# Kernel tuning notes

Hardware: AMD Instinct MI355X
Metric: run time of the kernel (lower is better)

## Reference

```python
import jax, jax.numpy as jnp
import numpy as np

N = 210          # sequence length (== module max_length cap)
DM = 2048        # input feature dim (major and minor)
DK = 1024        # key/query dim
DV = 1024        # value dim
K_CLIP = 32      # relative-position clipping distance


def _make_table(n, k):
    # table[i, j] = clip(j - i, -k, k) + k  (Shaw-style relative position index)
    rel = np.arange(n)[None, :] - np.arange(n)[:, None]
    return jnp.asarray(np.clip(rel, -k, k) + k, dtype=jnp.int32)


def setup_inputs() -> dict:
    key = jax.random.key(0)
    ks = jax.random.split(key, 7)
    X_major = jax.random.normal(ks[0], (N, DM), dtype=jnp.float32)
    X_minor = jax.random.normal(ks[1], (N, DM), dtype=jnp.float32)
    # Linear weights stored as [in, out] for x @ W
    s = 0.02
    Wq = jax.random.normal(ks[2], (DM, DK), dtype=jnp.float32) * s
    Wk = jax.random.normal(ks[3], (DM, DK), dtype=jnp.float32) * s
    Wv = jax.random.normal(ks[4], (DM, DV), dtype=jnp.float32) * s
    Wo = jax.random.normal(ks[5], (DV, DV), dtype=jnp.float32) * s
    wk = jax.random.normal(ks[6], (2 * K_CLIP + 1, DK), dtype=jnp.float32) * s
    table = _make_table(N, K_CLIP)
    return {"X_major": X_major, "X_minor": X_minor, "Wq": Wq, "Wk": Wk,
            "Wv": Wv, "Wo": Wo, "wk": wk, "table": table}


def reference(X_major, X_minor, Wq, Wk, Wv, Wo, wk, table):
    n = X_major.shape[0]
    scale = 1.0 / jnp.sqrt(jnp.asarray(Wq.shape[1], X_major.dtype))
    Q = X_major @ Wq                     # [n, dk]
    K = X_minor @ Wk                     # [n, dk]
    V = X_minor @ Wv                     # [n, dv]
    Qs = Q * scale
    S = Qs @ K.T                         # [n, n] content scores
    Rk = wk[table[:n, :n]]               # [n, n, dk] gathered rel-pos reps
    Sr = jnp.einsum('id,ijd->ij', Qs, Rk)  # [n, n] relative scores
    A = jax.nn.softmax(S + Sr, axis=-1)  # [n, n]
    Y = (A @ V) @ Wo                     # [n, dv]
    return (Y, A)
```

## Files before the change

kernel.cpp:

```cpp
#include <hip/hip_runtime.h>

typedef short bf16x8 __attribute__((ext_vector_type(8)));
typedef float f32x4 __attribute__((ext_vector_type(4)));

#define MFMA16(a, b, c) __builtin_amdgcn_mfma_f32_16x16x32_bf16(a, b, c, 0, 0, 0)

__device__ inline short f2bf(float f) {
  unsigned u = __builtin_bit_cast(unsigned, f);
  u += 0x7FFFu + ((u >> 16) & 1u);
  return (short)(u >> 16);
}
__device__ inline unsigned pack2(float lo, float hi) {
  unsigned a = __builtin_bit_cast(unsigned, lo) + 0x8000u;
  unsigned b = __builtin_bit_cast(unsigned, hi) + 0x8000u;
  return __builtin_amdgcn_perm(b, a, 0x07060302u);
}

__device__ inline void async_cp16(const void* g, void* l) {
  __builtin_amdgcn_global_load_lds(
      (const __attribute__((address_space(1))) unsigned int*)g,
      (__attribute__((address_space(3))) unsigned int*)l, 16, 0, 0);
}

#define SWZ(r, c) ((((r) << 4) + ((c) ^ ((r) & 7))) << 3)


__global__ __launch_bounds__(256) void k_prep(const float* __restrict__ xmaj,
                                              const float* __restrict__ xmin,
                                              const float* __restrict__ wkin,
                                              const float* __restrict__ Wq,
                                              const float* __restrict__ Wk,
                                              const float* __restrict__ Wv,
                                              const float* __restrict__ Wo,
                                              short* __restrict__ xmaj_bf,
                                              short* __restrict__ xmin_bf,
                                              short* __restrict__ kwb,
                                              short* __restrict__ wqt,
                                              short* __restrict__ wkt,
                                              short* __restrict__ wvt,
                                              short* __restrict__ wot) {
  __shared__ short tile[64][72];
  int b = blockIdx.x, t = threadIdx.x;
  if (b < 512) {
    int idx = b * 256 + t;
    if (idx < 107520) {
      float4 v = ((const float4*)xmaj)[idx];
      ((uint2*)xmaj_bf)[idx] = make_uint2(pack2(v.x, v.y), pack2(v.z, v.w));
      float4 u = ((const float4*)xmin)[idx];
      ((uint2*)xmin_bf)[idx] = make_uint2(pack2(u.x, u.y), pack2(u.z, u.w));
    }
    if (idx < 16640) {
      float4 v = ((const float4*)wkin)[idx];
      ((uint2*)(kwb + 210 * 1024))[idx] = make_uint2(pack2(v.x, v.y), pack2(v.z, v.w));
    }
    if (idx < 1664) ((uint4*)(kwb + 275 * 1024))[idx] = make_uint4(0, 0, 0, 0);
    return;
  }
  const float* W;
  short* Wt;
  int kt, nt, dstK;
  if (b < 2048) {
    int wi = (b - 512) >> 9, tl = (b - 512) & 511;
    W = wi == 0 ? Wq : (wi == 1 ? Wk : Wv);
    Wt = wi == 0 ? wqt : (wi == 1 ? wkt : wvt);
    kt = tl >> 4; nt = tl & 15; dstK = 2048;
  } else {
    int tl = b - 2048;
    W = Wo; Wt = wot; kt = tl >> 4; nt = tl & 15; dstK = 1024;
  }
  int k0 = kt * 64, n0 = nt * 64;
  int kp = t >> 4, nl4 = (t & 15) * 4;
  for (int h = 0; h < 2; ++h) {
    int kpp = kp + h * 16;
    const float* g = W + (size_t)(k0 + 2 * kpp) * 1024 + n0 + nl4;
    float4 u = *(const float4*)g;
    float4 v = *(const float4*)(g + 1024);
    *(unsigned*)&tile[nl4 + 0][2 * kpp] = pack2(u.x, v.x);
    *(unsigned*)&tile[nl4 + 1][2 * kpp] = pack2(u.y, v.y);
    *(unsigned*)&tile[nl4 + 2][2 * kpp] = pack2(u.z, v.z);
    *(unsigned*)&tile[nl4 + 3][2 * kpp] = pack2(u.w, v.w);
  }
  __syncthreads();
  int nl = t >> 2, cq = t & 3;
  for (int h = 0; h < 2; ++h) {
    int c = cq + h * 4;
    *(uint4*)(Wt + (size_t)(n0 + nl) * dstK + k0 + c * 8) = *(const uint4*)&tile[nl][c * 8];
  }
}

__global__ __launch_bounds__(256, 1) void k_qkv(const short* __restrict__ xmaj,
                                                const short* __restrict__ xmin,
                                                const short* __restrict__ wqt,
                                                const short* __restrict__ wkt,
                                                const short* __restrict__ wvt,
                                                short* __restrict__ qs,
                                                short* __restrict__ kwb,
                                                short* __restrict__ vt) {
  __shared__ short As[64 * 128];
  __shared__ short Bs[64 * 128];
  int b = blockIdx.x, t = threadIdx.x;
  int x = b & 7, s = b >> 3;
  int ntile = x * 6 + (s >> 2), mtile = s & 3;
  int nn0 = ntile * 64;
  int mat = nn0 >> 10, ncol0 = nn0 & 1023, m0 = mtile * 64;
  const short* A = (mat == 0) ? xmaj : xmin;
  const short* Bt = (mat == 0) ? wqt : (mat == 1 ? wkt : wvt);
  int lane = t & 63, w = t >> 6;
  int wm = w >> 1, wn = w & 1;
  int l15 = lane & 15, l4 = lane >> 4;
  f32x4 acc[2][2] = {};

  for (int k0 = 0; k0 < 2048; k0 += 128) {
    __syncthreads();
#pragma unroll
    for (int j = 0; j < 4; ++j) {
      int sj = t + j * 256;
      int r = sj >> 4, cg = (sj & 15) ^ (r & 7);
      async_cp16(A + (size_t)(m0 + r) * 2048 + k0 + cg * 8, &As[(w * 64 + j * 256) * 8]);
    }
#pragma unroll
    for (int j = 0; j < 4; ++j) {
      int sj = t + j * 256;
      int r = sj >> 4, cg = (sj & 15) ^ (r & 7);
      async_cp16(Bt + (size_t)(ncol0 + r) * 2048 + k0 + cg * 8, &Bs[(w * 64 + j * 256) * 8]);
    }
    __syncthreads();
#pragma unroll
    for (int kk = 0; kk < 4; ++kk) {
      int c = kk * 4 + l4;
      int ra0 = wm * 32 + l15, ra1 = ra0 + 16;
      int rb0 = wn * 32 + l15, rb1 = rb0 + 16;
      bf16x8 a0 = *(const bf16x8*)&As[SWZ(ra0, c)];
      bf16x8 a1 = *(const bf16x8*)&As[SWZ(ra1, c)];
      bf16x8 b0 = *(const bf16x8*)&Bs[SWZ(rb0, c)];
      bf16x8 b1 = *(const bf16x8*)&Bs[SWZ(rb1, c)];
      acc[0][0] = MFMA16(a0, b0, acc[0][0]);
      acc[0][1] = MFMA16(a0, b1, acc[0][1]);
      acc[1][0] = MFMA16(a1, b0, acc[1][0]);
      acc[1][1] = MFMA16(a1, b1, acc[1][1]);
    }
  }

  if (mat < 2) {
    float scale = (mat == 0) ? 0.03125f : 1.0f;
    short* dst = (mat == 0) ? qs : kwb;
#pragma unroll
    for (int mi = 0; mi < 2; ++mi)
#pragma unroll
      for (int ni = 0; ni < 2; ++ni) {
        int r0 = m0 + wm * 32 + mi * 16 + l4 * 4;
        int c = ncol0 + wn * 32 + ni * 16 + l15;
        for (int j = 0; j < 4; ++j) {
          int r = r0 + j;
          if (r < 210) dst[r * 1024 + c] = f2bf(acc[mi][ni][j] * scale);
        }
      }
  } else {
    __syncthreads();
#pragma unroll
    for (int mi = 0; mi < 2; ++mi)
#pragma unroll
      for (int ni = 0; ni < 2; ++ni) {
        int nl = wn * 32 + ni * 16 + l15;
        int ml0 = wm * 32 + mi * 16 + l4 * 4;
        for (int j = 0; j < 4; ++j) As[nl * 72 + ml0 + j] = f2bf(acc[mi][ni][j]);
      }
    __syncthreads();
    for (int h = 0; h < 2; ++h) {
      int idx = t + h * 256;
      int nl = idx >> 3, c8 = idx & 7;
      int mg0 = m0 + c8 * 8;
      short* dstp = vt + (ncol0 + nl) * 256 + mg0;
      if (mg0 + 8 <= 210) {
        *(uint4*)dstp = *(const uint4*)&As[nl * 72 + c8 * 8];
      } else {
        for (int e = 0; e < 8; ++e)
          if (mg0 + e < 210) dstp[e] = As[nl * 72 + c8 * 8 + e];
      }
    }
  }
}

__global__ __launch_bounds__(256, 1) void k_sprime(const short* __restrict__ qs,
                                                   const short* __restrict__ kwb,
                                                   float* __restrict__ Sp) {
  __shared__ short As[32 * 128];
  __shared__ short Bs[64 * 128];
  int n0 = blockIdx.x * 64, m0 = blockIdx.y * 32;
  int t = threadIdx.x, lane = t & 63, w = t >> 6;
  int l15 = lane & 15, l4 = lane >> 4;
  f32x4 acc[2] = {};

  for (int k0 = 0; k0 < 1024; k0 += 128) {
    __syncthreads();
#pragma unroll
    for (int j = 0; j < 2; ++j) {
      int sj = t + j * 256;
      int r = sj >> 4, cg = (sj & 15) ^ (r & 7);
      async_cp16(qs + (size_t)(m0 + r) * 1024 + k0 + cg * 8, &As[(w * 64 + j * 256) * 8]);
    }
#pragma unroll
    for (int j = 0; j < 4; ++j) {
      int sj = t + j * 256;
      int r = sj >> 4, cg = (sj & 15) ^ (r & 7);
      async_cp16(kwb + (size_t)(n0 + r) * 1024 + k0 + cg * 8, &Bs[(w * 64 + j * 256) * 8]);
    }
    __syncthreads();
#pragma unroll
    for (int kk = 0; kk < 4; ++kk) {
      int c = kk * 4 + l4;
      int rb = w * 16 + l15;
      bf16x8 a0 = *(const bf16x8*)&As[SWZ(l15, c)];
      bf16x8 a1 = *(const bf16x8*)&As[SWZ(16 + l15, c)];
      bf16x8 bb = *(const bf16x8*)&Bs[SWZ(rb, c)];
      acc[0] = MFMA16(a0, bb, acc[0]);
      acc[1] = MFMA16(a1, bb, acc[1]);
    }
  }
#pragma unroll
  for (int mi = 0; mi < 2; ++mi) {
    int r0 = m0 + mi * 16 + l4 * 4;
    int col = n0 + w * 16 + l15;
    for (int j = 0; j < 4; ++j) Sp[(r0 + j) * 320 + col] = acc[mi][j];
  }
}

__global__ __launch_bounds__(256) void k_softmax(const float* __restrict__ Sp,
                                                 const int* __restrict__ table,
                                                 short* __restrict__ Abf,
                                                 float* __restrict__ outA) {
  int i = blockIdx.x, t = threadIdx.x;
  if (i >= 210) {
    Abf[i * 256 + t] = 0;
    return;
  }
  __shared__ float srow[288];
  __shared__ float red[4];
  for (int j = t; j < 288; j += 256) srow[j] = Sp[i * 320 + j];
  __syncthreads();
  float logit = -1e30f;
  if (t < 210) {
    int tb = table[i * 210 + t];
    logit = srow[t] + srow[210 + tb];
  }
  float m = logit;
  for (int o = 32; o; o >>= 1) m = fmaxf(m, __shfl_xor(m, o));
  if ((t & 63) == 0) red[t >> 6] = m;
  __syncthreads();
  m = fmaxf(fmaxf(red[0], red[1]), fmaxf(red[2], red[3]));
  float e = (t < 210) ? __expf(logit - m) : 0.0f;
  float s = e;
  for (int o = 32; o; o >>= 1) s += __shfl_xor(s, o);
  __syncthreads();
  if ((t & 63) == 0) red[t >> 6] = s;
  __syncthreads();
  s = red[0] + red[1] + red[2] + red[3];
  float a = e / s;
  Abf[i * 256 + t] = (t < 210) ? f2bf(a) : (short)0;
  if (t < 210) outA[i * 210 + t] = a;
}

__global__ __launch_bounds__(256, 1) void k_av(const short* __restrict__ Abf,
                                               const short* __restrict__ vt,
                                               short* __restrict__ av) {
  __shared__ short As[64 * 128];
  __shared__ short Bs[64 * 128];
  int n0 = blockIdx.x * 64, m0 = blockIdx.y * 64;
  int t = threadIdx.x, lane = t & 63, w = t >> 6;
  int wm = w >> 1, wn = w & 1;
  int l15 = lane & 15, l4 = lane >> 4;
  f32x4 acc[2][2] = {};

  for (int k0 = 0; k0 < 256; k0 += 128) {
    __syncthreads();
#pragma unroll
    for (int j = 0; j < 4; ++j) {
      int sj = t + j * 256;
      int r = sj >> 4, cg = (sj & 15) ^ (r & 7);
      async_cp16(Abf + (size_t)(m0 + r) * 256 + k0 + cg * 8, &As[(w * 64 + j * 256) * 8]);
      async_cp16(vt + (size_t)(n0 + r) * 256 + k0 + cg * 8, &Bs[(w * 64 + j * 256) * 8]);
    }
    __syncthreads();
#pragma unroll
    for (int kk = 0; kk < 4; ++kk) {
      int c = kk * 4 + l4;
      int ra0 = wm * 32 + l15, ra1 = ra0 + 16;
      int rb0 = wn * 32 + l15, rb1 = rb0 + 16;
      bf16x8 a0 = *(const bf16x8*)&As[SWZ(ra0, c)];
      bf16x8 a1 = *(const bf16x8*)&As[SWZ(ra1, c)];
      bf16x8 b0 = *(const bf16x8*)&Bs[SWZ(rb0, c)];
      bf16x8 b1 = *(const bf16x8*)&Bs[SWZ(rb1, c)];
      acc[0][0] = MFMA16(a0, b0, acc[0][0]);
      acc[0][1] = MFMA16(a0, b1, acc[0][1]);
      acc[1][0] = MFMA16(a1, b0, acc[1][0]);
      acc[1][1] = MFMA16(a1, b1, acc[1][1]);
    }
  }
#pragma unroll
  for (int mi = 0; mi < 2; ++mi)
#pragma unroll
    for (int ni = 0; ni < 2; ++ni) {
      int r0 = m0 + wm * 32 + mi * 16 + l4 * 4;
      int c = n0 + wn * 32 + ni * 16 + l15;
      for (int j = 0; j < 4; ++j) {
        int r = r0 + j;
        if (r < 210) av[r * 1024 + c] = f2bf(acc[mi][ni][j]);
      }
    }
}

__global__ __launch_bounds__(256, 1) void k_y(const short* __restrict__ av,
                                              const short* __restrict__ wot,
                                              float* __restrict__ outY) {
  __shared__ short As[64 * 128];
  __shared__ short Bs[64 * 128];
  int n0 = blockIdx.x * 64, m0 = blockIdx.y * 64;
  int t = threadIdx.x, lane = t & 63, w = t >> 6;
  int wm = w >> 1, wn = w & 1;
  int l15 = lane & 15, l4 = lane >> 4;
  f32x4 acc[2][2] = {};

  for (int k0 = 0; k0 < 1024; k0 += 128) {
    __syncthreads();
#pragma unroll
    for (int j = 0; j < 4; ++j) {
      int sj = t + j * 256;
      int r = sj >> 4, cg = (sj & 15) ^ (r & 7);
      async_cp16(av + (size_t)(m0 + r) * 1024 + k0 + cg * 8, &As[(w * 64 + j * 256) * 8]);
      async_cp16(wot + (size_t)(n0 + r) * 1024 + k0 + cg * 8, &Bs[(w * 64 + j * 256) * 8]);
    }
    __syncthreads();
#pragma unroll
    for (int kk = 0; kk < 4; ++kk) {
      int c = kk * 4 + l4;
      int ra0 = wm * 32 + l15, ra1 = ra0 + 16;
      int rb0 = wn * 32 + l15, rb1 = rb0 + 16;
      bf16x8 a0 = *(const bf16x8*)&As[SWZ(ra0, c)];
      bf16x8 a1 = *(const bf16x8*)&As[SWZ(ra1, c)];
      bf16x8 b0 = *(const bf16x8*)&Bs[SWZ(rb0, c)];
      bf16x8 b1 = *(const bf16x8*)&Bs[SWZ(rb1, c)];
      acc[0][0] = MFMA16(a0, b0, acc[0][0]);
      acc[0][1] = MFMA16(a0, b1, acc[0][1]);
      acc[1][0] = MFMA16(a1, b0, acc[1][0]);
      acc[1][1] = MFMA16(a1, b1, acc[1][1]);
    }
  }
#pragma unroll
  for (int mi = 0; mi < 2; ++mi)
#pragma unroll
    for (int ni = 0; ni < 2; ++ni) {
      int r0 = m0 + wm * 32 + mi * 16 + l4 * 4;
      int c = n0 + wn * 32 + ni * 16 + l15;
      for (int j = 0; j < 4; ++j) {
        int r = r0 + j;
        if (r < 210) outY[r * 1024 + c] = acc[mi][ni][j];
      }
    }
}

extern "C" void kernel_launch(void* const* d_in, const int* in_sizes, int n_in,
                              void* d_out, int out_size, void* d_ws, size_t ws_size,
                              hipStream_t stream) {
  const float* Xmaj = (const float*)d_in[0];
  const float* Xmin = (const float*)d_in[1];
  const float* Wq = (const float*)d_in[2];
  const float* Wk = (const float*)d_in[3];
  const float* Wv = (const float*)d_in[4];
  const float* Wo = (const float*)d_in[5];
  const float* wk = (const float*)d_in[6];
  const int* table = (const int*)d_in[7];

  char* ws = (char*)d_ws;
  short* xmaj_bf = (short*)(ws + 0);
  short* xmin_bf = (short*)(ws + 1048576);
  short* qs = (short*)(ws + 2097152);
  short* kwb = (short*)(ws + 2621440);
  short* vt = (short*)(ws + 3276800);
  short* Abf = (short*)(ws + 3801088);
  short* av = (short*)(ws + 3932160);
  float* Sp = (float*)(ws + 4456448);
  short* wqt = (short*)(ws + 4743168);
  short* wkt = (short*)(ws + 8937472);
  short* wvt = (short*)(ws + 13131776);
  short* wot = (short*)(ws + 17326080);

  float* outY = (float*)d_out;
  float* outA = (float*)d_out + 215040;

  k_prep<<<2304, 256, 0, stream>>>(Xmaj, Xmin, wk, Wq, Wk, Wv, Wo,
                                   xmaj_bf, xmin_bf, kwb, wqt, wkt, wvt, wot);
  k_qkv<<<192, 256, 0, stream>>>(xmaj_bf, xmin_bf, wqt, wkt, wvt, qs, kwb, vt);
  k_sprime<<<dim3(5, 7), 256, 0, stream>>>(qs, kwb, Sp);
  k_softmax<<<256, 256, 0, stream>>>(Sp, table, Abf, outA);
  k_av<<<dim3(16, 4), 256, 0, stream>>>(Abf, vt, av);
  k_y<<<dim3(16, 4), 256, 0, stream>>>(av, wot, outY);
}
```

Measured before the change: 127.0 us.

## Fuse all stages into one cooperative persistent kernel with grid syncs

Replaces the six separate kernels with one cooperative kernel of 192 blocks that runs prep, QKV GEMM, scores+softmax, A@V and the output projection, separated by grid-wide syncs. The score GEMM and softmax are merged per 32-row block so scores stay in shared memory instead of going through a global buffer. This is meant to remove kernel launch overhead and inter-kernel gaps. In exchange, the weight conversion/transpose stage runs on far fewer blocks, and later stages leave most blocks idle at barriers.

Result: slower. 257.1 us (+102.4%).

```diff
diff --git a/kernel.cpp b/kernel.cpp
--- a/kernel.cpp
+++ b/kernel.cpp
@@ -1,4 +1,7 @@
 #include <hip/hip_runtime.h>
+#include <hip/hip_cooperative_groups.h>
+
+namespace cg = cooperative_groups;
 
 typedef short bf16x8 __attribute__((ext_vector_type(8)));
 typedef float f32x4 __attribute__((ext_vector_type(4)));
@@ -15,347 +18,352 @@
   unsigned b = __builtin_bit_cast(unsigned, hi) + 0x8000u;
   return __builtin_amdgcn_perm(b, a, 0x07060302u);
 }
-
 __device__ inline void async_cp16(const void* g, void* l) {
   __builtin_amdgcn_global_load_lds(
       (const __attribute__((address_space(1))) unsigned int*)g,
       (__attribute__((address_space(3))) unsigned int*)l, 16, 0, 0);
 }
-
 #define SWZ(r, c) ((((r) << 4) + ((c) ^ ((r) & 7))) << 3)
 
 
-__global__ __launch_bounds__(256) void k_prep(const float* __restrict__ xmaj,
-                                              const float* __restrict__ xmin,
-                                              const float* __restrict__ wkin,
-                                              const float* __restrict__ Wq,
-                                              const float* __restrict__ Wk,
-                                              const float* __restrict__ Wv,
-                                              const float* __restrict__ Wo,
-                                              short* __restrict__ xmaj_bf,
-                                              short* __restrict__ xmin_bf,
-                                              short* __restrict__ kwb,
-                                              short* __restrict__ wqt,
-                                              short* __restrict__ wkt,
-                                              short* __restrict__ wvt,
-                                              short* __restrict__ wot) {
-  __shared__ short tile[64][72];
+__global__ __launch_bounds__(256, 1) void k_fused(const float* __restrict__ xmajf,
+                                                  const float* __restrict__ xminf,
+                                                  const float* __restrict__ Wqf,
+                                                  const float* __restrict__ Wkf,
+                                                  const float* __restrict__ Wvf,
+                                                  const float* __restrict__ Wof,
+                                                  const float* __restrict__ wkin,
+                                                  const int* __restrict__ table,
+                                                  char* __restrict__ ws,
+                                                  float* __restrict__ dout) {
+  __shared__ char smem[90112];
+  cg::grid_group gg = cg::this_grid();
   int b = blockIdx.x, t = threadIdx.x;
-  if (b < 512) {
-    int idx = b * 256 + t;
-    if (idx < 107520) {
-      float4 v = ((const float4*)xmaj)[idx];
-      ((uint2*)xmaj_bf)[idx] = make_uint2(pack2(v.x, v.y), pack2(v.z, v.w));
-      float4 u = ((const float4*)xmin)[idx];
-      ((uint2*)xmin_bf)[idx] = make_uint2(pack2(u.x, u.y), pack2(u.z, u.w));
-    }
-    if (idx < 16640) {
-      float4 v = ((const float4*)wkin)[idx];
-      ((uint2*)(kwb + 210 * 1024))[idx] = make_uint2(pack2(v.x, v.y), pack2(v.z, v.w));
-    }
-    if (idx < 1664) ((uint4*)(kwb + 275 * 1024))[idx] = make_uint4(0, 0, 0, 0);
-    return;
-  }
-  const float* W;
-  short* Wt;
-  int kt, nt, dstK;
-  if (b < 2048) {
-    int wi = (b - 512) >> 9, tl = (b - 512) & 511;
-    W = wi == 0 ? Wq : (wi == 1 ? Wk : Wv);
-    Wt = wi == 0 ? wqt : (wi == 1 ? wkt : wvt);
-    kt = tl >> 4; nt = tl & 15; dstK = 2048;
-  } else {
-    int tl = b - 2048;
-    W = Wo; Wt = wot; kt = tl >> 4; nt = tl & 15; dstK = 1024;
-  }
-  int k0 = kt * 64, n0 = nt * 64;
-  int kp = t >> 4, nl4 = (t & 15) * 4;
-  for (int h = 0; h < 2; ++h) {
-    int kpp = kp + h * 16;
-    const float* g = W + (size_t)(k0 + 2 * kpp) * 1024 + n0 + nl4;
-    float4 u = *(const float4*)g;
-    float4 v = *(const float4*)(g + 1024);
-    *(unsigned*)&tile[nl4 + 0][2 * kpp] = pack2(u.x, v.x);
-    *(unsigned*)&tile[nl4 + 1][2 * kpp] = pack2(u.y, v.y);
-    *(unsigned*)&tile[nl4 + 2][2 * kpp] = pack2(u.z, v.z);
-    *(unsigned*)&tile[nl4 + 3][2 * kpp] = pack2(u.w, v.w);
-  }
-  __syncthreads();
-  int nl = t >> 2, cq = t & 3;
-  for (int h = 0; h < 2; ++h) {
-    int c = cq + h * 4;
-    *(uint4*)(Wt + (size_t)(n0 + nl) * dstK + k0 + c * 8) = *(const uint4*)&tile[nl][c * 8];
-  }
-}
-
-__global__ __launch_bounds__(256, 1) void k_qkv(const short* __restrict__ xmaj,
-                                                const short* __restrict__ xmin,
-                                                const short* __restrict__ wqt,
-                                                const short* __restrict__ wkt,
-                                                const short* __restrict__ wvt,
-                                                short* __restrict__ qs,
-                                                short* __restrict__ kwb,
-                                                short* __restrict__ vt) {
-  __shared__ short As[64 * 128];
-  __shared__ short Bs[64 * 128];
-  int b = blockIdx.x, t = threadIdx.x;
-  int x = b & 7, s = b >> 3;
-  int ntile = x * 6 + (s >> 2), mtile = s & 3;
-  int nn0 = ntile * 64;
-  int mat = nn0 >> 10, ncol0 = nn0 & 1023, m0 = mtile * 64;
-  const short* A = (mat == 0) ? xmaj : xmin;
-  const short* Bt = (mat == 0) ? wqt : (mat == 1 ? wkt : wvt);
   int lane = t & 63, w = t >> 6;
-  int wm = w >> 1, wn = w & 1;
   int l15 = lane & 15, l4 = lane >> 4;
-  f32x4 acc[2][2] = {};
-
-  for (int k0 = 0; k0 < 2048; k0 += 128) {
+
+  short* xmaj_bf = (short*)(ws);
+  short* xmin_bf = (short*)(ws + 1048576);
+  short* qs = (short*)(ws + 2097152);
+  short* kwb = (short*)(ws + 2621440);
+  short* vt = (short*)(ws + 3276800);
+  short* Abf = (short*)(ws + 3801088);
+  short* av = (short*)(ws + 3932160);
+  short* wqt = (short*)(ws + 4743168);
+  short* wkt = (short*)(ws + 8937472);
+  short* wvt = (short*)(ws + 13131776);
+  short* wot = (short*)(ws + 17326080);
+  float* outY = dout;
+  float* outA = dout + 215040;
+
+  {
+    for (int i = b * 256 + t; i < 107520; i += 49152) {
+      float4 v = ((const float4*)xmajf)[i];
+      ((uint2*)xmaj_bf)[i] = make_uint2(pack2(v.x, v.y), pack2(v.z, v.w));
+      float4 u = ((const float4*)xminf)[i];
+      ((uint2*)xmin_bf)[i] = make_uint2(pack2(u.x, u.y), pack2(u.z, u.w));
+    }
+    for (int i = b * 256 + t; i < 16640; i += 49152) {
+      float4 v = ((const float4*)wkin)[i];
+      ((uint2*)(kwb + 210 * 1024))[i] = make_uint2(pack2(v.x, v.y), pack2(v.z, v.w));
+    }
+    for (int i = b * 256 + t; i < 1664; i += 49152)
+      ((uint4*)(kwb + 275 * 1024))[i] = make_uint4(0, 0, 0, 0);
+
+    short(*tile)[72] = (short(*)[72])smem;
+    int kp = t >> 4, nl4 = (t & 15) * 4;
+    int nl = t >> 2, cq = t & 3;
+    for (int tid = b; tid < 1792; tid += 192) {
+      const float* W;
+      short* Wt;
+      int kt, nt, dstK;
+      if (tid < 1536) {
+        int wi = tid >> 9, tl = tid & 511;
+        W = wi == 0 ? Wqf : (wi == 1 ? Wkf : Wvf);
+        Wt = wi == 0 ? wqt : (wi == 1 ? wkt : wvt);
+        kt = tl >> 4; nt = tl & 15; dstK = 2048;
+      } else {
+        int tl = tid - 1536;
+        W = Wof; Wt = wot; kt = tl >> 4; nt = tl & 15; dstK = 1024;
+      }
+      int k0 = kt * 64, n0 = nt * 64;
+      __syncthreads();
+#pragma unroll
+      for (int h = 0; h < 2; ++h) {
+        int kpp = kp + h * 16;
+        const float* g = W + (size_t)(k0 + 2 * kpp) * 1024 + n0 + nl4;
+        float4 u = *(const float4*)g;
+        float4 v = *(const float4*)(g + 1024);
+        *(unsigned*)&tile[nl4 + 0][2 * kpp] = pack2(u.x, v.x);
+        *(unsigned*)&tile[nl4 + 1][2 * kpp] = pack2(u.y, v.y);
+        *(unsigned*)&tile[nl4 + 2][2 * kpp] = pack2(u.z, v.z);
+        *(unsigned*)&tile[nl4 + 3][2 * kpp] = pack2(u.w, v.w);
+      }
+      __syncthreads();
+#pragma unroll
+      for (int h = 0; h < 2; ++h) {
+        int c = cq + h * 4;
+        *(uint4*)(Wt + (size_t)(n0 + nl) * dstK + k0 + c * 8) = *(const uint4*)&tile[nl][c * 8];
+      }
+    }
+  }
+  gg.sync();
+
+  {
+    short* As = (short*)smem;
+    short* Bs = (short*)(smem + 16384);
+    int x = b & 7, s = b >> 3;
+    int ntile = x * 6 + (s >> 2), mtile = s & 3;
+    int nn0 = ntile * 64;
+    int mat = nn0 >> 10, ncol0 = nn0 & 1023, m0 = mtile * 64;
+    const short* A = (mat == 0) ? xmaj_bf : xmin_bf;
+    const short* Bt = (mat == 0) ? wqt : (mat == 1 ? wkt : wvt);
+    int wm = w >> 1, wn = w & 1;
+    f32x4 acc[2][2] = {};
+
+    for (int k0 = 0; k0 < 2048; k0 += 128) {
+      __syncthreads();
+#pragma unroll
+      for (int j = 0; j < 4; ++j) {
+        int sj = t + j * 256;
+        int r = sj >> 4, cg2 = (sj & 15) ^ (r & 7);
+        async_cp16(A + (size_t)(m0 + r) * 2048 + k0 + cg2 * 8, &As[(w * 64 + j * 256) * 8]);
+      }
+#pragma unroll
+      for (int j = 0; j < 4; ++j) {
+        int sj = t + j * 256;
+        int r = sj >> 4, cg2 = (sj & 15) ^ (r & 7);
+        async_cp16(Bt + (size_t)(ncol0 + r) * 2048 + k0 + cg2 * 8, &Bs[(w * 64 + j * 256) * 8]);
+      }
+      __syncthreads();
+#pragma unroll
+      for (int kk = 0; kk < 4; ++kk) {
+        int c = kk * 4 + l4;
+        int ra0 = wm * 32 + l15, ra1 = ra0 + 16;
+        int rb0 = wn * 32 + l15, rb1 = rb0 + 16;
+        bf16x8 a0 = *(const bf16x8*)&As[SWZ(ra0, c)];
+        bf16x8 a1 = *(const bf16x8*)&As[SWZ(ra1, c)];
+        bf16x8 b0 = *(const bf16x8*)&Bs[SWZ(rb0, c)];
+        bf16x8 b1 = *(const bf16x8*)&Bs[SWZ(rb1, c)];
+        acc[0][0] = MFMA16(a0, b0, acc[0][0]);
+        acc[0][1] = MFMA16(a0, b1, acc[0][1]);
+        acc[1][0] = MFMA16(a1, b0, acc[1][0]);
+        acc[1][1] = MFMA16(a1, b1, acc[1][1]);
+      }
+    }
+
+    if (mat < 2) {
+      float scale = (mat == 0) ? 0.03125f : 1.0f;
+      short* dst = (mat == 0) ? qs : kwb;
+#pragma unroll
+      for (int mi = 0; mi < 2; ++mi)
+#pragma unroll
+        for (int ni = 0; ni < 2; ++ni) {
+          int r0 = m0 + wm * 32 + mi * 16 + l4 * 4;
+          int c = ncol0 + wn * 32 + ni * 16 + l15;
+          for (int j = 0; j < 4; ++j) {
+            int r = r0 + j;
+            if (r < 210) dst[r * 1024 + c] = f2bf(acc[mi][ni][j] * scale);
+          }
+        }
+    } else {
+      __syncthreads();
+#pragma unroll
+      for (int mi = 0; mi < 2; ++mi)
+#pragma unroll
+        for (int ni = 0; ni < 2; ++ni) {
+          int nl = wn * 32 + ni * 16 + l15;
+          int ml0 = wm * 32 + mi * 16 + l4 * 4;
+          for (int j = 0; j < 4; ++j) As[nl * 72 + ml0 + j] = f2bf(acc[mi][ni][j]);
+        }
+      __syncthreads();
+      for (int h = 0; h < 2; ++h) {
+        int idx = t + h * 256;
+        int nl = idx >> 3, c8 = idx & 7;
+        int mg0 = m0 + c8 * 8;
+        short* dstp = vt + (ncol0 + nl) * 256 + mg0;
+        if (mg0 + 8 <= 210) {
+          *(uint4*)dstp = *(const uint4*)&As[nl * 72 + c8 * 8];
+        } else {
+          for (int e = 0; e < 8; ++e)
+            if (mg0 + e < 210) dstp[e] = As[nl * 72 + c8 * 8 + e];
+        }
+      }
+    }
+  }
+  gg.sync();
+
+#define SST 292
+  if (b < 7) {
+    short* As2 = (short*)smem;
+    short* Bs2 = (short*)(smem + 8192);
+    float* Ssh = (float*)(smem + 8192);
+    int m0 = b * 32;
+    f32x4 acc[2][5] = {};
+
+    for (int k0 = 0; k0 < 1024; k0 += 128) {
+      __syncthreads();
+#pragma unroll
+      for (int j = 0; j < 2; ++j) {
+        int sj = t + j * 256;
+        int r = sj >> 4, cg2 = (sj & 15) ^ (r & 7);
+        async_cp16(qs + (size_t)(m0 + r) * 1024 + k0 + cg2 * 8, &As2[(w * 64 + j * 256) * 8]);
+      }
+#pragma unroll
+      for (int j = 0; j < 20; ++j) {
+        int sj = t + j * 256;
+        int r = sj >> 4, cg2 = (sj & 15) ^ (r & 7);
+        async_cp16(kwb + (size_t)r * 1024 + k0 + cg2 * 8, &Bs2[(w * 64 + j * 256) * 8]);
+      }
+      __syncthreads();
+#pragma unroll
+      for (int kk = 0; kk < 4; ++kk) {
+        int c = kk * 4 + l4;
+        bf16x8 a0 = *(const bf16x8*)&As2[SWZ(l15, c)];
+        bf16x8 a1 = *(const bf16x8*)&As2[SWZ(16 + l15, c)];
+#pragma unroll
+        for (int ni = 0; ni < 5; ++ni) {
+          bf16x8 bb = *(const bf16x8*)&Bs2[SWZ(w * 80 + ni * 16 + l15, c)];
+          acc[0][ni] = MFMA16(a0, bb, acc[0][ni]);
+          acc[1][ni] = MFMA16(a1, bb, acc[1][ni]);
+        }
+      }
+    }
     __syncthreads();
 #pragma unroll
-    for (int j = 0; j < 4; ++j) {
-      int sj = t + j * 256;
-      int r = sj >> 4, cg = (sj & 15) ^ (r & 7);
-      async_cp16(A + (size_t)(m0 + r) * 2048 + k0 + cg * 8, &As[(w * 64 + j * 256) * 8]);
-    }
-#pragma unroll
-    for (int j = 0; j < 4; ++j) {
-      int sj = t + j * 256;
-      int r = sj >> 4, cg = (sj & 15) ^ (r & 7);
-      async_cp16(Bt + (size_t)(ncol0 + r) * 2048 + k0 + cg * 8, &Bs[(w * 64 + j * 256) * 8]);
-    }
+    for (int mi = 0; mi < 2; ++mi)
+#pragma unroll
+      for (int ni = 0; ni < 5; ++ni) {
+        int col = w * 80 + ni * 16 + l15;
+        if (col < 288) {
+          int r0 = mi * 16 + l4 * 4;
+          for (int jj = 0; jj < 4; ++jj) Ssh[(r0 + jj) * SST + col] = acc[mi][ni][jj];
+        }
+      }
     __syncthreads();
-#pragma unroll
-    for (int kk = 0; kk < 4; ++kk) {
-      int c = kk * 4 + l4;
-      int ra0 = wm * 32 + l15, ra1 = ra0 + 16;
-      int rb0 = wn * 32 + l15, rb1 = rb0 + 16;
-      bf16x8 a0 = *(const bf16x8*)&As[SWZ(ra0, c)];
-      bf16x8 a1 = *(const bf16x8*)&As[SWZ(ra1, c)];
-      bf16x8 b0 = *(const bf16x8*)&Bs[SWZ(rb0, c)];
-      bf16x8 b1 = *(const bf16x8*)&Bs[SWZ(rb1, c)];
-      acc[0][0] = MFMA16(a0, b0, acc[0][0]);
-      acc[0][1] = MFMA16(a0, b1, acc[0][1]);
-      acc[1][0] = MFMA16(a1, b0, acc[1][0]);
-      acc[1][1] = MFMA16(a1, b1, acc[1][1]);
-    }
-  }
-
-  if (mat < 2) {
-    float scale = (mat == 0) ? 0.03125f : 1.0f;
-    short* dst = (mat == 0) ? qs : kwb;
+
+    int r = t >> 3, c = t & 7;
+    int row = m0 + r;
+    float* Sr = Ssh + r * SST;
+    if (row < 210) {
+      const int* tr = table + row * 210;
+      float mx = -1e30f;
+      for (int j = c; j < 210; j += 8) {
+        float lg = Sr[j] + Sr[210 + tr[j]];
+        Sr[j] = lg;
+        mx = fmaxf(mx, lg);
+      }
+      for (int o = 4; o; o >>= 1) mx = fmaxf(mx, __shfl_xor(mx, o, 8));
+      float sum = 0.0f;
+      for (int j = c; j < 210; j += 8) {
+        float e = __expf(Sr[j] - mx);
+        Sr[j] = e;
+        sum += e;
+      }
+      for (int o = 4; o; o >>= 1) sum += __shfl_xor(sum, o, 8);
+      float inv = 1.0f / sum;
+      for (int j = c; j < 210; j += 8) {
+        float a = Sr[j] * inv;
+        outA[row * 210 + j] = a;
+        Abf[row * 256 + j] = f2bf(a);
+      }
+      for (int j = 210 + c; j < 256; j += 8) Abf[row * 256 + j] = 0;
+    } else {
+      for (int j = c; j < 256; j += 8) Abf[row * 256 + j] = 0;
+    }
+  } else if (b == 7) {
+    for (int i = t; i < 1472; i += 256) ((uint4*)(Abf + 210 * 256))[i] = make_uint4(0, 0, 0, 0);
+  }
+  gg.sync();
+
+  if (b < 64) {
+    short* As = (short*)smem;
+    short* Bs = (short*)(smem + 16384);
+    int n0 = (b & 15) * 64, m0 = (b >> 4) * 64;
+    int wm = w >> 1, wn = w & 1;
+    f32x4 acc[2][2] = {};
+    for (int k0 = 0; k0 < 256; k0 += 128) {
+      __syncthreads();
+#pragma unroll
+      for (int j = 0; j < 4; ++j) {
+        int sj = t + j * 256;
+        int r = sj >> 4, cg2 = (sj & 15) ^ (r & 7);
+        async_cp16(Abf + (size_t)(m0 + r) * 256 + k0 + cg2 * 8, &As[(w * 64 + j * 256) * 8]);
+        async_cp16(vt + (size_t)(n0 + r) * 256 + k0 + cg2 * 8, &Bs[(w * 64 + j * 256) * 8]);
+      }
+      __syncthreads();
+#pragma unroll
+      for (int kk = 0; kk < 4; ++kk) {
+        int c = kk * 4 + l4;
+        int ra0 = wm * 32 + l15, ra1 = ra0 + 16;
+        int rb0 = wn * 32 + l15, rb1 = rb0 + 16;
+        bf16x8 a0 = *(const bf16x8*)&As[SWZ(ra0, c)];
+        bf16x8 a1 = *(const bf16x8*)&As[SWZ(ra1, c)];
+        bf16x8 b0 = *(const bf16x8*)&Bs[SWZ(rb0, c)];
+        bf16x8 b1 = *(const bf16x8*)&Bs[SWZ(rb1, c)];
+        acc[0][0] = MFMA16(a0, b0, acc[0][0]);
+        acc[0][1] = MFMA16(a0, b1, acc[0][1]);
+        acc[1][0] = MFMA16(a1, b0, acc[1][0]);
+        acc[1][1] = MFMA16(a1, b1, acc[1][1]);
+      }
+    }
 #pragma unroll
     for (int mi = 0; mi < 2; ++mi)
 #pragma unroll
       for (int ni = 0; ni < 2; ++ni) {
         int r0 = m0 + wm * 32 + mi * 16 + l4 * 4;
-        int c = ncol0 + wn * 32 + ni * 16 + l15;
+        int c = n0 + wn * 32 + ni * 16 + l15;
         for (int j = 0; j < 4; ++j) {
           int r = r0 + j;
-          if (r < 210) dst[r * 1024 + c] = f2bf(acc[mi][ni][j] * scale);
-        }
-      }
-  } else {
-    __syncthreads();
+          if (r < 210) av[r * 1024 + c] = f2bf(acc[mi][ni][j]);
+        }
+      }
+  }
+  gg.sync();
+
+  if (b < 64) {
+    short* As = (short*)smem;
+    short* Bs = (short*)(smem + 16384);
+    int n0 = (b & 15) * 64, m0 = (b >> 4) * 64;
+    int wm = w >> 1, wn = w & 1;
+    f32x4 acc[2][2] = {};
+    for (int k0 = 0; k0 < 1024; k0 += 128) {
+      __syncthreads();
+#pragma unroll
+      for (int j = 0; j < 4; ++j) {
+        int sj = t + j * 256;
+        int r = sj >> 4, cg2 = (sj & 15) ^ (r & 7);
+        async_cp16(av + (size_t)(m0 + r) * 1024 + k0 + cg2 * 8, &As[(w * 64 + j * 256) * 8]);
+        async_cp16(wot + (size_t)(n0 + r) * 1024 + k0 + cg2 * 8, &Bs[(w * 64 + j * 256) * 8]);
+      }
+      __syncthreads();
+#pragma unroll
+      for (int kk = 0; kk < 4; ++kk) {
+        int c = kk * 4 + l4;
+        int ra0 = wm * 32 + l15, ra1 = ra0 + 16;
+        int rb0 = wn * 32 + l15, rb1 = rb0 + 16;
+        bf16x8 a0 = *(const bf16x8*)&As[SWZ(ra0, c)];
+        bf16x8 a1 = *(const bf16x8*)&As[SWZ(ra1, c)];
+        bf16x8 b0 = *(const bf16x8*)&Bs[SWZ(rb0, c)];
+        bf16x8 b1 = *(const bf16x8*)&Bs[SWZ(rb1, c)];
+        acc[0][0] = MFMA16(a0, b0, acc[0][0]);
+        acc[0][1] = MFMA16(a0, b1, acc[0][1]);
+        acc[1][0] = MFMA16(a1, b0, acc[1][0]);
+        acc[1][1] = MFMA16(a1, b1, acc[1][1]);
+      }
+    }
 #pragma unroll
     for (int mi = 0; mi < 2; ++mi)
 #pragma unroll
       for (int ni = 0; ni < 2; ++ni) {
-        int nl = wn * 32 + ni * 16 + l15;
-        int ml0 = wm * 32 + mi * 16 + l4 * 4;
-        for (int j = 0; j < 4; ++j) As[nl * 72 + ml0 + j] = f2bf(acc[mi][ni][j]);
-      }
-    __syncthreads();
-    for (int h = 0; h < 2; ++h) {
-      int idx = t + h * 256;
-      int nl = idx >> 3, c8 = idx & 7;
-      int mg0 = m0 + c8 * 8;
-      short* dstp = vt + (ncol0 + nl) * 256 + mg0;
-      if (mg0 + 8 <= 210) {
-        *(uint4*)dstp = *(const uint4*)&As[nl * 72 + c8 * 8];
-      } else {
-        for (int e = 0; e < 8; ++e)
-          if (mg0 + e < 210) dstp[e] = As[nl * 72 + c8 * 8 + e];
-      }
-    }
-  }
-}
-
-__global__ __launch_bounds__(256, 1) void k_sprime(const short* __restrict__ qs,
-                                                   const short* __restrict__ kwb,
-                                                   float* __restrict__ Sp) {
-  __shared__ short As[32 * 128];
-  __shared__ short Bs[64 * 128];
-  int n0 = blockIdx.x * 64, m0 = blockIdx.y * 32;
-  int t = threadIdx.x, lane = t & 63, w = t >> 6;
-  int l15 = lane & 15, l4 = lane >> 4;
-  f32x4 acc[2] = {};
-
-  for (int k0 = 0; k0 < 1024; k0 += 128) {
-    __syncthreads();
-#pragma unroll
-    for (int j = 0; j < 2; ++j) {
-      int sj = t + j * 256;
-      int r = sj >> 4, cg = (sj & 15) ^ (r & 7);
-      async_cp16(qs + (size_t)(m0 + r) * 1024 + k0 + cg * 8, &As[(w * 64 + j * 256) * 8]);
-    }
-#pragma unroll
-    for (int j = 0; j < 4; ++j) {
-      int sj = t + j * 256;
-      int r = sj >> 4, cg = (sj & 15) ^ (r & 7);
-      async_cp16(kwb + (size_t)(n0 + r) * 1024 + k0 + cg * 8, &Bs[(w * 64 + j * 256) * 8]);
-    }
-    __syncthreads();
-#pragma unroll
-    for (int kk = 0; kk < 4; ++kk) {
-      int c = kk * 4 + l4;
-      int rb = w * 16 + l15;
-      bf16x8 a0 = *(const bf16x8*)&As[SWZ(l15, c)];
-      bf16x8 a1 = *(const bf16x8*)&As[SWZ(16 + l15, c)];
-      bf16x8 bb = *(const bf16x8*)&Bs[SWZ(rb, c)];
-      acc[0] = MFMA16(a0, bb, acc[0]);
-      acc[1] = MFMA16(a1, bb, acc[1]);
-    }
-  }
-#pragma unroll
-  for (int mi = 0; mi < 2; ++mi) {
-    int r0 = m0 + mi * 16 + l4 * 4;
-    int col = n0 + w * 16 + l15;
-    for (int j = 0; j < 4; ++j) Sp[(r0 + j) * 320 + col] = acc[mi][j];
-  }
-}
-
-__global__ __launch_bounds__(256) void k_softmax(const float* __restrict__ Sp,
-                                                 const int* __restrict__ table,
-                                                 short* __restrict__ Abf,
-                                                 float* __restrict__ outA) {
-  int i = blockIdx.x, t = threadIdx.x;
-  if (i >= 210) {
-    Abf[i * 256 + t] = 0;
-    return;
-  }
-  __shared__ float srow[288];
-  __shared__ float red[4];
-  for (int j = t; j < 288; j += 256) srow[j] = Sp[i * 320 + j];
-  __syncthreads();
-  float logit = -1e30f;
-  if (t < 210) {
-    int tb = table[i * 210 + t];
-    logit = srow[t] + srow[210 + tb];
-  }
-  float m = logit;
-  for (int o = 32; o; o >>= 1) m = fmaxf(m, __shfl_xor(m, o));
-  if ((t & 63) == 0) red[t >> 6] = m;
-  __syncthreads();
-  m = fmaxf(fmaxf(red[0], red[1]), fmaxf(red[2], red[3]));
-  float e = (t < 210) ? __expf(logit - m) : 0.0f;
-  float s = e;
-  for (int o = 32; o; o >>= 1) s += __shfl_xor(s, o);
-  __syncthreads();
-  if ((t & 63) == 0) red[t >> 6] = s;
-  __syncthreads();
-  s = red[0] + red[1] + red[2] + red[3];
-  float a = e / s;
-  Abf[i * 256 + t] = (t < 210) ? f2bf(a) : (short)0;
-  if (t < 210) outA[i * 210 + t] = a;
-}
-
-__global__ __launch_bounds__(256, 1) void k_av(const short* __restrict__ Abf,
-                                               const short* __restrict__ vt,
-                                               short* __restrict__ av) {
-  __shared__ short As[64 * 128];
-  __shared__ short Bs[64 * 128];
-  int n0 = blockIdx.x * 64, m0 = blockIdx.y * 64;
-  int t = threadIdx.x, lane = t & 63, w = t >> 6;
-  int wm = w >> 1, wn = w & 1;
-  int l15 = lane & 15, l4 = lane >> 4;
-  f32x4 acc[2][2] = {};
-
-  for (int k0 = 0; k0 < 256; k0 += 128) {
-    __syncthreads();
-#pragma unroll
-    for (int j = 0; j < 4; ++j) {
-      int sj = t + j * 256;
-      int r = sj >> 4, cg = (sj & 15) ^ (r & 7);
-      async_cp16(Abf + (size_t)(m0 + r) * 256 + k0 + cg * 8, &As[(w * 64 + j * 256) * 8]);
-      async_cp16(vt + (size_t)(n0 + r) * 256 + k0 + cg * 8, &Bs[(w * 64 + j * 256) * 8]);
-    }
-    __syncthreads();
-#pragma unroll
-    for (int kk = 0; kk < 4; ++kk) {
-      int c = kk * 4 + l4;
-      int ra0 = wm * 32 + l15, ra1 = ra0 + 16;
-      int rb0 = wn * 32 + l15, rb1 = rb0 + 16;
-      bf16x8 a0 = *(const bf16x8*)&As[SWZ(ra0, c)];
-      bf16x8 a1 = *(const bf16x8*)&As[SWZ(ra1, c)];
-      bf16x8 b0 = *(const bf16x8*)&Bs[SWZ(rb0, c)];
-      bf16x8 b1 = *(const bf16x8*)&Bs[SWZ(rb1, c)];
-      acc[0][0] = MFMA16(a0, b0, acc[0][0]);
-      acc[0][1] = MFMA16(a0, b1, acc[0][1]);
-      acc[1][0] = MFMA16(a1, b0, acc[1][0]);
-      acc[1][1] = MFMA16(a1, b1, acc[1][1]);
-    }
-  }
-#pragma unroll
-  for (int mi = 0; mi < 2; ++mi)
-#pragma unroll
-    for (int ni = 0; ni < 2; ++ni) {
-      int r0 = m0 + wm * 32 + mi * 16 + l4 * 4;
-      int c = n0 + wn * 32 + ni * 16 + l15;
-      for (int j = 0; j < 4; ++j) {
-        int r = r0 + j;
-        if (r < 210) av[r * 1024 + c] = f2bf(acc[mi][ni][j]);
-      }
-    }
-}
-
-__global__ __launch_bounds__(256, 1) void k_y(const short* __restrict__ av,
-                                              const short* __restrict__ wot,
-                                              float* __restrict__ outY) {
-  __shared__ short As[64 * 128];
-  __shared__ short Bs[64 * 128];
-  int n0 = blockIdx.x * 64, m0 = blockIdx.y * 64;
-  int t = threadIdx.x, lane = t & 63, w = t >> 6;
-  int wm = w >> 1, wn = w & 1;
-  int l15 = lane & 15, l4 = lane >> 4;
-  f32x4 acc[2][2] = {};
-
-  for (int k0 = 0; k0 < 1024; k0 += 128) {
-    __syncthreads();
-#pragma unroll
-    for (int j = 0; j < 4; ++j) {
-      int sj = t + j * 256;
-      int r = sj >> 4, cg = (sj & 15) ^ (r & 7);
-      async_cp16(av + (size_t)(m0 + r) * 1024 + k0 + cg * 8, &As[(w * 64 + j * 256) * 8]);
-      async_cp16(wot + (size_t)(n0 + r) * 1024 + k0 + cg * 8, &Bs[(w * 64 + j * 256) * 8]);
-    }
-    __syncthreads();
-#pragma unroll
-    for (int kk = 0; kk < 4; ++kk) {
-      int c = kk * 4 + l4;
-      int ra0 = wm * 32 + l15, ra1 = ra0 + 16;
-      int rb0 = wn * 32 + l15, rb1 = rb0 + 16;
-      bf16x8 a0 = *(const bf16x8*)&As[SWZ(ra0, c)];
-      bf16x8 a1 = *(const bf16x8*)&As[SWZ(ra1, c)];
-      bf16x8 b0 = *(const bf16x8*)&Bs[SWZ(rb0, c)];
-      bf16x8 b1 = *(const bf16x8*)&Bs[SWZ(rb1, c)];
-      acc[0][0] = MFMA16(a0, b0, acc[0][0]);
-      acc[0][1] = MFMA16(a0, b1, acc[0][1]);
-      acc[1][0] = MFMA16(a1, b0, acc[1][0]);
-      acc[1][1] = MFMA16(a1, b1, acc[1][1]);
-    }
-  }
-#pragma unroll
-  for (int mi = 0; mi < 2; ++mi)
-#pragma unroll
-    for (int ni = 0; ni < 2; ++ni) {
-      int r0 = m0 + wm * 32 + mi * 16 + l4 * 4;
-      int c = n0 + wn * 32 + ni * 16 + l15;
-      for (int j = 0; j < 4; ++j) {
-        int r = r0 + j;
-        if (r < 210) outY[r * 1024 + c] = acc[mi][ni][j];
-      }
-    }
+        int r0 = m0 + wm * 32 + mi * 16 + l4 * 4;
+        int c = n0 + wn * 32 + ni * 16 + l15;
+        for (int j = 0; j < 4; ++j) {
+          int r = r0 + j;
+          if (r < 210) outY[r * 1024 + c] = acc[mi][ni][j];
+        }
+      }
+  }
 }
 
 extern "C" void kernel_launch(void* const* d_in, const int* in_sizes, int n_in,
@@ -369,29 +377,10 @@
   const float* Wo = (const float*)d_in[5];
   const float* wk = (const float*)d_in[6];
   const int* table = (const int*)d_in[7];
-
-  char* ws = (char*)d_ws;
-  short* xmaj_bf = (short*)(ws + 0);
-  short* xmin_bf = (short*)(ws + 1048576);
-  short* qs = (short*)(ws + 2097152);
-  short* kwb = (short*)(ws + 2621440);
-  short* vt = (short*)(ws + 3276800);
-  short* Abf = (short*)(ws + 3801088);
-  short* av = (short*)(ws + 3932160);
-  float* Sp = (float*)(ws + 4456448);
-  short* wqt = (short*)(ws + 4743168);
-  short* wkt = (short*)(ws + 8937472);
-  short* wvt = (short*)(ws + 13131776);
-  short* wot = (short*)(ws + 17326080);
-
-  float* outY = (float*)d_out;
-  float* outA = (float*)d_out + 215040;
-
-  k_prep<<<2304, 256, 0, stream>>>(Xmaj, Xmin, wk, Wq, Wk, Wv, Wo,
-                                   xmaj_bf, xmin_bf, kwb, wqt, wkt, wvt, wot);
-  k_qkv<<<192, 256, 0, stream>>>(xmaj_bf, xmin_bf, wqt, wkt, wvt, qs, kwb, vt);
-  k_sprime<<<dim3(5, 7), 256, 0, stream>>>(qs, kwb, Sp);
-  k_softmax<<<256, 256, 0, stream>>>(Sp, table, Abf, outA);
-  k_av<<<dim3(16, 4), 256, 0, stream>>>(Abf, vt, av);
-  k_y<<<dim3(16, 4), 256, 0, stream>>>(av, wot, outY);
-}
+  char* wsp = (char*)d_ws;
+  float* outp = (float*)d_out;
+
+  void* args[] = {(void*)&Xmaj, (void*)&Xmin, (void*)&Wq, (void*)&Wk, (void*)&Wv,
+                  (void*)&Wo,   (void*)&wk,   (void*)&table, (void*)&wsp, (void*)&outp};
+  hipLaunchCooperativeKernel((void*)k_fused, dim3(192), dim3(256), args, 0, stream);
+}
```

## Fuse score GEMM and softmax into one attention kernel

Applied to the files above, without the earlier changes.

Merges the S' GEMM (Q against K and relative-position keys) with the row softmax into a single kernel. Each of 7 blocks computes a full 32x320 score strip in LDS and applies the softmax there, so the Sp buffer round trip through global memory and one kernel launch go away. Zeroing of the padding rows of Abf moves into the prep kernel. The cost is far less parallelism: 7 blocks instead of 35 for the GEMM, and each block must stream all of kwb by itself.

After: 146.1 us. 15.0% more time.

```diff
diff --git a/kernel.cpp b/kernel.cpp
--- a/kernel.cpp
+++ b/kernel.cpp
@@ -35,6 +35,7 @@
                                               short* __restrict__ xmaj_bf,
                                               short* __restrict__ xmin_bf,
                                               short* __restrict__ kwb,
+                                              short* __restrict__ Abf,
                                               short* __restrict__ wqt,
                                               short* __restrict__ wkt,
                                               short* __restrict__ wvt,
@@ -54,6 +55,8 @@
       ((uint2*)(kwb + 210 * 1024))[idx] = make_uint2(pack2(v.x, v.y), pack2(v.z, v.w));
     }
     if (idx < 1664) ((uint4*)(kwb + 275 * 1024))[idx] = make_uint4(0, 0, 0, 0);
+    if (idx < 1472)
+      ((uint4*)(Abf + 210 * 256))[idx] = make_uint4(0, 0, 0, 0);
     return;
   }
   const float* W;
@@ -181,83 +184,91 @@
   }
 }
 
-__global__ __launch_bounds__(256, 1) void k_sprime(const short* __restrict__ qs,
-                                                   const short* __restrict__ kwb,
-                                                   float* __restrict__ Sp) {
-  __shared__ short As[32 * 128];
-  __shared__ short Bs[64 * 128];
-  int n0 = blockIdx.x * 64, m0 = blockIdx.y * 32;
-  int t = threadIdx.x, lane = t & 63, w = t >> 6;
-  int l15 = lane & 15, l4 = lane >> 4;
-  f32x4 acc[2] = {};
-
-  for (int k0 = 0; k0 < 1024; k0 += 128) {
-    __syncthreads();
-#pragma unroll
-    for (int j = 0; j < 2; ++j) {
-      int sj = t + j * 256;
-      int r = sj >> 4, cg = (sj & 15) ^ (r & 7);
-      async_cp16(qs + (size_t)(m0 + r) * 1024 + k0 + cg * 8, &As[(w * 64 + j * 256) * 8]);
-    }
-#pragma unroll
-    for (int j = 0; j < 4; ++j) {
-      int sj = t + j * 256;
-      int r = sj >> 4, cg = (sj & 15) ^ (r & 7);
-      async_cp16(kwb + (size_t)(n0 + r) * 1024 + k0 + cg * 8, &Bs[(w * 64 + j * 256) * 8]);
-    }
-    __syncthreads();
-#pragma unroll
-    for (int kk = 0; kk < 4; ++kk) {
-      int c = kk * 4 + l4;
-      int rb = w * 16 + l15;
-      bf16x8 a0 = *(const bf16x8*)&As[SWZ(l15, c)];
-      bf16x8 a1 = *(const bf16x8*)&As[SWZ(16 + l15, c)];
-      bf16x8 bb = *(const bf16x8*)&Bs[SWZ(rb, c)];
-      acc[0] = MFMA16(a0, bb, acc[0]);
-      acc[1] = MFMA16(a1, bb, acc[1]);
-    }
-  }
-#pragma unroll
-  for (int mi = 0; mi < 2; ++mi) {
-    int r0 = m0 + mi * 16 + l4 * 4;
-    int col = n0 + w * 16 + l15;
-    for (int j = 0; j < 4; ++j) Sp[(r0 + j) * 320 + col] = acc[mi][j];
-  }
-}
-
-__global__ __launch_bounds__(256) void k_softmax(const float* __restrict__ Sp,
+#define SST 292
+__global__ __launch_bounds__(256, 1) void k_attn(const short* __restrict__ qs,
+                                                 const short* __restrict__ kwb,
                                                  const int* __restrict__ table,
                                                  short* __restrict__ Abf,
                                                  float* __restrict__ outA) {
-  int i = blockIdx.x, t = threadIdx.x;
-  if (i >= 210) {
-    Abf[i * 256 + t] = 0;
-    return;
-  }
-  __shared__ float srow[288];
-  __shared__ float red[4];
-  for (int j = t; j < 288; j += 256) srow[j] = Sp[i * 320 + j];
+  __shared__ short As2[32 * 128];
+  __shared__ short Bs2[320 * 128];
+  float* Ssh = (float*)Bs2;
+  int b = blockIdx.x, t = threadIdx.x;
+  int lane = t & 63, w = t >> 6;
+  int l15 = lane & 15, l4 = lane >> 4;
+  int m0 = b * 32;
+  f32x4 acc[2][5] = {};
+
+  for (int k0 = 0; k0 < 1024; k0 += 128) {
+    __syncthreads();
+#pragma unroll
+    for (int j = 0; j < 2; ++j) {
+      int sj = t + j * 256;
+      int r = sj >> 4, cg = (sj & 15) ^ (r & 7);
+      async_cp16(qs + (size_t)(m0 + r) * 1024 + k0 + cg * 8, &As2[(w * 64 + j * 256) * 8]);
+    }
+#pragma unroll
+    for (int j = 0; j < 20; ++j) {
+      int sj = t + j * 256;
+      int r = sj >> 4, cg = (sj & 15) ^ (r & 7);
+      async_cp16(kwb + (size_t)r * 1024 + k0 + cg * 8, &Bs2[(w * 64 + j * 256) * 8]);
+    }
+    __syncthreads();
+#pragma unroll
+    for (int kk = 0; kk < 4; ++kk) {
+      int c = kk * 4 + l4;
+      bf16x8 a0 = *(const bf16x8*)&As2[SWZ(l15, c)];
+      bf16x8 a1 = *(const bf16x8*)&As2[SWZ(16 + l15, c)];
+#pragma unroll
+      for (int ni = 0; ni < 5; ++ni) {
+        bf16x8 bb = *(const bf16x8*)&Bs2[SWZ(w * 80 + ni * 16 + l15, c)];
+        acc[0][ni] = MFMA16(a0, bb, acc[0][ni]);
+        acc[1][ni] = MFMA16(a1, bb, acc[1][ni]);
+      }
+    }
+  }
   __syncthreads();
-  float logit = -1e30f;
-  if (t < 210) {
-    int tb = table[i * 210 + t];
-    logit = srow[t] + srow[210 + tb];
-  }
-  float m = logit;
-  for (int o = 32; o; o >>= 1) m = fmaxf(m, __shfl_xor(m, o));
-  if ((t & 63) == 0) red[t >> 6] = m;
+#pragma unroll
+  for (int mi = 0; mi < 2; ++mi)
+#pragma unroll
+    for (int ni = 0; ni < 5; ++ni) {
+      int col = w * 80 + ni * 16 + l15;
+      if (col < 288) {
+        int r0 = mi * 16 + l4 * 4;
+        for (int jj = 0; jj < 4; ++jj) Ssh[(r0 + jj) * SST + col] = acc[mi][ni][jj];
+      }
+    }
   __syncthreads();
-  m = fmaxf(fmaxf(red[0], red[1]), fmaxf(red[2], red[3]));
-  float e = (t < 210) ? __expf(logit - m) : 0.0f;
-  float s = e;
-  for (int o = 32; o; o >>= 1) s += __shfl_xor(s, o);
-  __syncthreads();
-  if ((t & 63) == 0) red[t >> 6] = s;
-  __syncthreads();
-  s = red[0] + red[1] + red[2] + red[3];
-  float a = e / s;
-  Abf[i * 256 + t] = (t < 210) ? f2bf(a) : (short)0;
-  if (t < 210) outA[i * 210 + t] = a;
+
+  int r = t >> 3, c = t & 7;
+  int row = m0 + r;
+  float* Sr = Ssh + r * SST;
+  if (row < 210) {
+    const int* tr = table + row * 210;
+    float mx = -1e30f;
+    for (int j = c; j < 210; j += 8) {
+      float lg = Sr[j] + Sr[210 + tr[j]];
+      Sr[j] = lg;
+      mx = fmaxf(mx, lg);
+    }
+    for (int o = 4; o; o >>= 1) mx = fmaxf(mx, __shfl_xor(mx, o, 8));
+    float sum = 0.0f;
+    for (int j = c; j < 210; j += 8) {
+      float e = __expf(Sr[j] - mx);
+      Sr[j] = e;
+      sum += e;
+    }
+    for (int o = 4; o; o >>= 1) sum += __shfl_xor(sum, o, 8);
+    float inv = 1.0f / sum;
+    for (int j = c; j < 210; j += 8) {
+      float a = Sr[j] * inv;
+      outA[row * 210 + j] = a;
+      Abf[row * 256 + j] = f2bf(a);
+    }
+    for (int j = 210 + c; j < 256; j += 8) Abf[row * 256 + j] = 0;
+  } else {
+    for (int j = c; j < 256; j += 8) Abf[row * 256 + j] = 0;
+  }
 }
 
 __global__ __launch_bounds__(256, 1) void k_av(const short* __restrict__ Abf,
@@ -378,7 +389,6 @@
   short* vt = (short*)(ws + 3276800);
   short* Abf = (short*)(ws + 3801088);
   short* av = (short*)(ws + 3932160);
-  float* Sp = (float*)(ws + 4456448);
   short* wqt = (short*)(ws + 4743168);
   short* wkt = (short*)(ws + 8937472);
   short* wvt = (short*)(ws + 13131776);
@@ -388,10 +398,9 @@
   float* outA = (float*)d_out + 215040;
 
   k_prep<<<2304, 256, 0, stream>>>(Xmaj, Xmin, wk, Wq, Wk, Wv, Wo,
-                                   xmaj_bf, xmin_bf, kwb, wqt, wkt, wvt, wot);
+                                   xmaj_bf, xmin_bf, kwb, Abf, wqt, wkt, wvt, wot);
   k_qkv<<<192, 256, 0, stream>>>(xmaj_bf, xmin_bf, wqt, wkt, wvt, qs, kwb, vt);
-  k_sprime<<<dim3(5, 7), 256, 0, stream>>>(qs, kwb, Sp);
-  k_softmax<<<256, 256, 0, stream>>>(Sp, table, Abf, outA);
+  k_attn<<<7, 256, 0, stream>>>(qs, kwb, table, Abf, outA);
   k_av<<<dim3(16, 4), 256, 0, stream>>>(Abf, vt, av);
   k_y<<<dim3(16, 4), 256, 0, stream>>>(av, wot, outY);
 }
```
